# Optimization experiments

Measured on AMD Instinct MI355X. Metric: run time of the kernel, lower is better.

The kernel has to match this reference:

```python
import jax, jax.numpy as jnp
import numpy as np

N_QUBITS = 4
N_LAYERS = 2
BATCH = 524288


def _apply_1q(state, U, axis):
    # state: [B, 2,2,2,2]; U: [2,2] (shared) or [B,2,2] (per-sample); axis = wire index + 1
    s = jnp.moveaxis(state, axis, -1)
    if U.ndim == 3:
        s = jnp.einsum('bij,b...j->b...i', U, s)
    else:
        s = jnp.einsum('ij,...j->...i', U, s)
    return jnp.moveaxis(s, -1, axis)


def _apply_cz(state, a, b):
    # diagonal CZ: flip sign where both qubits are |1>
    sign = jnp.array([[1.0, 1.0], [1.0, -1.0]], dtype=state.dtype)
    shape = [1] * state.ndim
    shape[a] = 2
    shape[b] = 2
    return state * sign.reshape(shape)


def _quantum_expval(feats, w):
    # feats: [B, n_qubits] angles; w: [n_layers, n_qubits, 3] Rot params
    B = feats.shape[0]
    state = jnp.zeros((B,) + (2,) * N_QUBITS, jnp.complex64)
    state = state.at[(slice(None),) + (0,) * N_QUBITS].set(1.0)
    # per-sample RY embedding
    for i in range(N_QUBITS):
        c = jnp.cos(feats[:, i] * 0.5)
        s = jnp.sin(feats[:, i] * 0.5)
        U = jnp.stack([jnp.stack([c, -s], -1), jnp.stack([s, c], -1)], -2).astype(jnp.complex64)
        state = _apply_1q(state, U, i + 1)
    # variational layers: Rot(phi,theta,omega) = RZ(omega) RY(theta) RZ(phi), then CZ chain
    for l in range(N_LAYERS):
        for i in range(N_QUBITS):
            phi, theta, omega = w[l, i, 0], w[l, i, 1], w[l, i, 2]
            ct = jnp.cos(theta * 0.5)
            st = jnp.sin(theta * 0.5)
            U = jnp.stack([
                jnp.stack([jnp.exp(-0.5j * (phi + omega)) * ct, -jnp.exp(0.5j * (phi - omega)) * st]),
                jnp.stack([jnp.exp(-0.5j * (phi - omega)) * st, jnp.exp(0.5j * (phi + omega)) * ct]),
            ]).astype(jnp.complex64)
            state = _apply_1q(state, U, i + 1)
        for i in range(N_QUBITS - 1):
            state = _apply_cz(state, i + 1, i + 2)
    probs = jnp.square(jnp.abs(state))
    p = probs.sum(axis=tuple(range(2, N_QUBITS + 1)))  # marginal of wire 0 -> [B, 2]
    return (p[:, 0] - p[:, 1]).astype(jnp.float32)  # <Z_0>


def setup_inputs() -> dict:
    key = jax.random.key(0)
    ks = jax.random.split(key, 12)
    f = jnp.float32
    return {
        'text': jax.random.normal(ks[0], (BATCH, 16), f),
        'image': jax.random.normal(ks[1], (BATCH, 48), f),
        'tW1': jax.random.normal(ks[2], (16, 32), f) * 0.25,
        'tb1': jnp.zeros((32,), f),
        'tW2': jax.random.normal(ks[3], (32, N_QUBITS), f) * 0.18,
        'tb2': jnp.zeros((N_QUBITS,), f),
        'iW1': jax.random.normal(ks[4], (48, 64), f) * 0.14,
        'ib1': jnp.zeros((64,), f),
        'iW2': jax.random.normal(ks[5], (64, N_QUBITS), f) * 0.125,
        'ib2': jnp.zeros((N_QUBITS,), f),
        'qweights': jax.random.normal(ks[6], (N_LAYERS, N_QUBITS, 3), f),
        'cW1': jax.random.normal(ks[7], (1, 16), f),
        'cb1': jnp.zeros((16,), f),
        'cW2': jax.random.normal(ks[8], (16, 2), f) * 0.25,
        'cb2': jnp.zeros((2,), f),
    }


def reference(text, image, tW1, tb1, tW2, tb2, iW1, ib1, iW2, ib2, qweights, cW1, cb1, cW2, cb2):
    tf = jax.nn.relu(text @ tW1 + tb1) @ tW2 + tb2      # [B, 4]
    imf = jax.nn.relu(image @ iW1 + ib1) @ iW2 + ib2    # [B, 4]
    feats = (tf + imf) * 0.5                             # [B, 4]
    q = _quantum_expval(feats, qweights)                 # [B]
    h = jax.nn.relu(q[:, None] @ cW1 + cb1)              # [B, 16]
    return h @ cW2 + cb2                                 # [B, 2]
```

## Files before the change

### kernel.cpp

```cpp
#include <hip/hip_runtime.h>
#include <math.h>

#define NQ 4
#define NL 2

#define O_IMG 0
#define O_AS  12288
#define O_MRE 12544
#define O_MIM 12800
#define LDS_FLOATS 13056

__global__ __launch_bounds__(256, 4) void qnn_fused(
    const float* __restrict__ text, const float* __restrict__ image,
    const float* __restrict__ tW1, const float* __restrict__ tb1,
    const float* __restrict__ tW2, const float* __restrict__ tb2,
    const float* __restrict__ iW1, const float* __restrict__ ib1,
    const float* __restrict__ iW2, const float* __restrict__ ib2,
    const float* __restrict__ qw,
    const float* __restrict__ cW1, const float* __restrict__ cb1,
    const float* __restrict__ cW2, const float* __restrict__ cb2,
    float* __restrict__ out, int B)
{
    __shared__ __align__(16) float S[LDS_FLOATS];
    const int tid = threadIdx.x;

    {
        const int sbase = blockIdx.x * 256;
        #pragma unroll
        for (int j = 0; j < 12; ++j) {
            int flat = j * 256 + tid;
            int sl = flat / 12;
            int c  = flat - sl * 12;
            int sg = sbase + sl; if (sg >= B) sg = B - 1;
            float4 v = ((const float4*)image)[(size_t)sg * 12 + c];
            *(float4*)&S[O_IMG + sl * 48 + c * 4] = v;
        }
    }

    if (tid < 16) {
        const int j = tid;
        float re[16], im[16];
        #pragma unroll
        for (int b = 0; b < 16; ++b) { re[b] = (b == j) ? 1.f : 0.f; im[b] = 0.f; }
        for (int l = 0; l < NL; ++l) {
            for (int i = 0; i < NQ; ++i) {
                float phi   = qw[(l*NQ + i)*3 + 0];
                float theta = qw[(l*NQ + i)*3 + 1];
                float omega = qw[(l*NQ + i)*3 + 2];
                float ct, st; __sincosf(0.5f*theta, &st, &ct);
                float cap, sap, cam, sam;
                __sincosf(0.5f*(phi + omega), &sap, &cap);
                __sincosf(0.5f*(phi - omega), &sam, &cam);
                float u00r =  cap*ct, u00i = -sap*ct;
                float u01r = -cam*st, u01i = -sam*st;
                float u10r =  cam*st, u10i = -sam*st;
                float u11r =  cap*ct, u11i =  sap*ct;
                int mask = 1 << (3 - i);
                #pragma unroll
                for (int b = 0; b < 16; ++b) {
                    if (b & mask) continue;
                    int b1 = b | mask;
                    float a0r = re[b],  a0i = im[b];
                    float a1r = re[b1], a1i = im[b1];
                    re[b]  = u00r*a0r - u00i*a0i + u01r*a1r - u01i*a1i;
                    im[b]  = u00r*a0i + u00i*a0r + u01r*a1i + u01i*a1r;
                    re[b1] = u10r*a0r - u10i*a0i + u11r*a1r - u11i*a1i;
                    im[b1] = u10r*a0i + u10i*a0r + u11r*a1i + u11i*a1r;
                }
            }
            #pragma unroll
            for (int b = 0; b < 16; ++b) {
                float sgn = 1.f;
                if ((b & 0xC) == 0xC) sgn = -sgn;
                if ((b & 0x6) == 0x6) sgn = -sgn;
                if ((b & 0x3) == 0x3) sgn = -sgn;
                re[b] *= sgn; im[b] *= sgn;
            }
        }
        #pragma unroll
        for (int b = 0; b < 16; ++b) { S[O_MRE + j*16 + b] = re[b]; S[O_MIM + j*16 + b] = im[b]; }
    }
    __syncthreads();
    {
        int j = tid >> 4, k = tid & 15;
        float sacc = 0.f;
        #pragma unroll
        for (int b = 0; b < 16; ++b) {
            float sg = (b & 8) ? -1.f : 1.f;
            sacc += sg * (S[O_MRE + j*16 + b]*S[O_MRE + k*16 + b] +
                          S[O_MIM + j*16 + b]*S[O_MIM + k*16 + b]);
        }
        S[O_AS + tid] = sacc;
    }
    __syncthreads();

    const int s  = blockIdx.x * 256 + tid;
    const int cs = (s < B) ? s : (B - 1);

    float xt[16];
    {
        const float4* tg = (const float4*)(text + (size_t)cs * 16);
        #pragma unroll
        for (int k4 = 0; k4 < 4; ++k4) {
            float4 v = tg[k4];
            xt[4*k4] = v.x; xt[4*k4+1] = v.y; xt[4*k4+2] = v.z; xt[4*k4+3] = v.w;
        }
    }

    float f0 = ib2[0] + tb2[0];
    float f1 = ib2[1] + tb2[1];
    float f2 = ib2[2] + tb2[2];
    float f3 = ib2[3] + tb2[3];

    for (int g = 0; g < 2; ++g) {
        float acc[32];
        #pragma unroll
        for (int j = 0; j < 32; ++j) acc[j] = ib1[g*32 + j];
        #pragma unroll 2
        for (int k4 = 0; k4 < 12; ++k4) {
            float4 xv = *(const float4*)&S[O_IMG + tid*48 + k4*4];
            #pragma unroll
            for (int kk = 0; kk < 4; ++kk) {
                float e = (kk == 0) ? xv.x : (kk == 1) ? xv.y : (kk == 2) ? xv.z : xv.w;
                const float* wr = iW1 + (k4*4 + kk)*64 + g*32;
                #pragma unroll
                for (int j = 0; j < 32; ++j)
                    acc[j] = fmaf(e, wr[j], acc[j]);
            }
        }
        #pragma unroll
        for (int j = 0; j < 32; ++j) {
            float r = fmaxf(acc[j], 0.f);
            const float* w2 = iW2 + (g*32 + j)*4;
            f0 = fmaf(r, w2[0], f0); f1 = fmaf(r, w2[1], f1);
            f2 = fmaf(r, w2[2], f2); f3 = fmaf(r, w2[3], f3);
        }
    }

    for (int g = 0; g < 2; ++g) {
        float acc[16];
        #pragma unroll
        for (int j = 0; j < 16; ++j) acc[j] = tb1[g*16 + j];
        #pragma unroll 4
        for (int k = 0; k < 16; ++k) {
            const float* wr = tW1 + k*32 + g*16;
            float e = xt[k];
            #pragma unroll
            for (int j = 0; j < 16; ++j)
                acc[j] = fmaf(e, wr[j], acc[j]);
        }
        #pragma unroll
        for (int j = 0; j < 16; ++j) {
            float r = fmaxf(acc[j], 0.f);
            const float* w2 = tW2 + (g*16 + j)*4;
            f0 = fmaf(r, w2[0], f0); f1 = fmaf(r, w2[1], f1);
            f2 = fmaf(r, w2[2], f2); f3 = fmaf(r, w2[3], f3);
        }
    }

    float c0,s0v,c1,s1v,c2,s2v,c3,s3v;
    __sincosf(f0 * 0.25f, &s0v, &c0);
    __sincosf(f1 * 0.25f, &s1v, &c1);
    __sincosf(f2 * 0.25f, &s2v, &c2);
    __sincosf(f3 * 0.25f, &s3v, &c3);
    float p01[4] = { c0*c1, c0*s1v, s0v*c1, s0v*s1v };
    float p23[4] = { c2*c3, c2*s3v, s2v*c3, s2v*s3v };
    float psi[16];
    #pragma unroll
    for (int x = 0; x < 4; ++x)
        #pragma unroll
        for (int y = 0; y < 4; ++y)
            psi[x*4+y] = p01[x] * p23[y];

    float q = 0.f;
    #pragma unroll
    for (int j = 0; j < 16; ++j) {
        float row = 0.f;
        #pragma unroll
        for (int k4 = 0; k4 < 4; ++k4) {
            float4 a = *(const float4*)&S[O_AS + j*16 + k4*4];
            row = fmaf(a.x, psi[k4*4+0], row);
            row = fmaf(a.y, psi[k4*4+1], row);
            row = fmaf(a.z, psi[k4*4+2], row);
            row = fmaf(a.w, psi[k4*4+3], row);
        }
        q = fmaf(psi[j], row, q);
    }

    float o0 = cb2[0], o1 = cb2[1];
    #pragma unroll
    for (int j = 0; j < 16; ++j) {
        float h = fmaxf(fmaf(q, cW1[j], cb1[j]), 0.f);
        o0 = fmaf(h, cW2[j*2 + 0], o0);
        o1 = fmaf(h, cW2[j*2 + 1], o1);
    }
    if (s < B) ((float2*)out)[s] = make_float2(o0, o1);
}

extern "C" void kernel_launch(void* const* d_in, const int* in_sizes, int n_in,
                              void* d_out, int out_size, void* d_ws, size_t ws_size,
                              hipStream_t stream)
{
    const float* text  = (const float*)d_in[0];
    const float* image = (const float*)d_in[1];
    const float* tW1   = (const float*)d_in[2];
    const float* tb1   = (const float*)d_in[3];
    const float* tW2   = (const float*)d_in[4];
    const float* tb2   = (const float*)d_in[5];
    const float* iW1   = (const float*)d_in[6];
    const float* ib1   = (const float*)d_in[7];
    const float* iW2   = (const float*)d_in[8];
    const float* ib2   = (const float*)d_in[9];
    const float* qw    = (const float*)d_in[10];
    const float* cW1   = (const float*)d_in[11];
    const float* cb1   = (const float*)d_in[12];
    const float* cW2   = (const float*)d_in[13];
    const float* cb2   = (const float*)d_in[14];

    int B = in_sizes[0] / 16;
    int grid = (B + 255) / 256;

    qnn_fused<<<grid, 256, 0, stream>>>(
        text, image, tW1, tb1, tW2, tb2, iW1, ib1, iW2, ib2,
        qw, cW1, cb1, cW2, cb2, (float*)d_out, B);
}
```

Before: 268.5 us.

## Register-tile MLP across samples and hidden units with LDS-staged weights

Each block now handles 128 samples, and each thread computes a 4-sample by 8-hidden-unit register tile for the image MLP and a 4x4 tile for the text MLP. Weights, biases and padded input tiles are staged in LDS. Partial feature sums are reduced through LDS before half the threads run the quantum and head stages. The aim is to stop every thread streaming all weights from global/scalar memory and to raise FMA-to-load reuse. The cost is more LDS per block, an extra barrier, half the threads idle during the tail, and lower occupancy bounds.

```diff
diff --git a/kernel.cpp b/kernel.cpp
--- a/kernel.cpp
+++ b/kernel.cpp
@@ -4,13 +4,26 @@
 #define NQ 4
 #define NL 2
 
-#define O_IMG 0
-#define O_AS  12288
-#define O_MRE 12544
-#define O_MIM 12800
-#define LDS_FLOATS 13056
-
-__global__ __launch_bounds__(256, 4) void qnn_fused(
+#define O_XI   0
+#define O_XT   6272
+#define O_WI1  8448
+#define O_WI2  11520
+#define O_WT1  11776
+#define O_WT2  12288
+#define O_IB1  12416
+#define O_TB1  12480
+#define O_FB2  12512
+#define O_CW1  12516
+#define O_CB1  12532
+#define O_CW2  12548
+#define O_CB2  12580
+#define O_PT   12584
+#define O_AS   17704
+#define O_MRE  17960
+#define O_MIM  18216
+#define LDS_FLOATS 18472
+
+__global__ __launch_bounds__(256, 2) void qnn_fused(
     const float* __restrict__ text, const float* __restrict__ image,
     const float* __restrict__ tW1, const float* __restrict__ tb1,
     const float* __restrict__ tW2, const float* __restrict__ tb2,
@@ -23,18 +36,43 @@
 {
     __shared__ __align__(16) float S[LDS_FLOATS];
     const int tid = threadIdx.x;
-
-    {
-        const int sbase = blockIdx.x * 256;
-        #pragma unroll
-        for (int j = 0; j < 12; ++j) {
-            int flat = j * 256 + tid;
+    const int blk = blockIdx.x;
+
+    {
+        const float4* img4 = (const float4*)image;
+        #pragma unroll
+        for (int i = 0; i < 6; ++i) {
+            int flat = i * 256 + tid;
             int sl = flat / 12;
-            int c  = flat - sl * 12;
-            int sg = sbase + sl; if (sg >= B) sg = B - 1;
-            float4 v = ((const float4*)image)[(size_t)sg * 12 + c];
-            *(float4*)&S[O_IMG + sl * 48 + c * 4] = v;
-        }
+            int c4 = flat - sl * 12;
+            int sg = blk * 128 + sl; if (sg >= B) sg = B - 1;
+            float4 v = img4[(size_t)sg * 12 + c4];
+            float* d = &S[O_XI + sl * 49 + c4 * 4];
+            d[0] = v.x; d[1] = v.y; d[2] = v.z; d[3] = v.w;
+        }
+        const float4* txt4 = (const float4*)text;
+        #pragma unroll
+        for (int i = 0; i < 2; ++i) {
+            int flat = i * 256 + tid;
+            int sl = flat >> 2;
+            int c4 = flat & 3;
+            int sg = blk * 128 + sl; if (sg >= B) sg = B - 1;
+            float4 v = txt4[(size_t)sg * 4 + c4];
+            float* d = &S[O_XT + sl * 17 + c4 * 4];
+            d[0] = v.x; d[1] = v.y; d[2] = v.z; d[3] = v.w;
+        }
+        #pragma unroll
+        for (int i = 0; i < 12; ++i) S[O_WI1 + i*256 + tid] = iW1[i*256 + tid];
+        S[O_WI2 + tid] = iW2[tid];
+        #pragma unroll
+        for (int i = 0; i < 2; ++i) S[O_WT1 + i*256 + tid] = tW1[i*256 + tid];
+        if (tid < 128) S[O_WT2 + tid] = tW2[tid];
+        if (tid < 64)  S[O_IB1 + tid] = ib1[tid];
+        if (tid < 32)  S[O_TB1 + tid] = tb1[tid];
+        if (tid < 4)   S[O_FB2 + tid] = ib2[tid] + tb2[tid];
+        if (tid < 16) { S[O_CW1 + tid] = cW1[tid]; S[O_CB1 + tid] = cb1[tid]; }
+        if (tid < 32)  S[O_CW2 + tid] = cW2[tid];
+        if (tid < 2)   S[O_CB2 + tid] = cb2[tid];
     }
 
     if (tid < 16) {
@@ -81,6 +119,7 @@
         for (int b = 0; b < 16; ++b) { S[O_MRE + j*16 + b] = re[b]; S[O_MIM + j*16 + b] = im[b]; }
     }
     __syncthreads();
+
     {
         int j = tid >> 4, k = tid & 15;
         float sacc = 0.f;
@@ -92,109 +131,164 @@
         }
         S[O_AS + tid] = sacc;
     }
+
+    const int lane = tid & 63;
+    const int wave = tid >> 6;
+    const int hw   = lane >> 5;
+    const int l5   = lane & 31;
+
+    float part[4][4];
+    #pragma unroll
+    for (int r = 0; r < 4; ++r)
+        #pragma unroll
+        for (int o = 0; o < 4; ++o) part[r][o] = 0.f;
+
+    {
+        const int nb = (wave*2 + hw) * 8;
+        float acc[4][8];
+        #pragma unroll
+        for (int j = 0; j < 8; ++j) {
+            float bv = S[O_IB1 + nb + j];
+            acc[0][j] = bv; acc[1][j] = bv; acc[2][j] = bv; acc[3][j] = bv;
+        }
+        const float* x0p = &S[O_XI + (l5 +  0) * 49];
+        const float* x1p = &S[O_XI + (l5 + 32) * 49];
+        const float* x2p = &S[O_XI + (l5 + 64) * 49];
+        const float* x3p = &S[O_XI + (l5 + 96) * 49];
+        const float* wp  = &S[O_WI1 + nb];
+        #pragma unroll
+        for (int k = 0; k < 48; ++k) {
+            float x0 = x0p[k], x1 = x1p[k], x2 = x2p[k], x3 = x3p[k];
+            float4 wA = *(const float4*)&wp[k*64];
+            float4 wB = *(const float4*)&wp[k*64 + 4];
+            acc[0][0] = fmaf(x0, wA.x, acc[0][0]); acc[0][1] = fmaf(x0, wA.y, acc[0][1]);
+            acc[0][2] = fmaf(x0, wA.z, acc[0][2]); acc[0][3] = fmaf(x0, wA.w, acc[0][3]);
+            acc[0][4] = fmaf(x0, wB.x, acc[0][4]); acc[0][5] = fmaf(x0, wB.y, acc[0][5]);
+            acc[0][6] = fmaf(x0, wB.z, acc[0][6]); acc[0][7] = fmaf(x0, wB.w, acc[0][7]);
+            acc[1][0] = fmaf(x1, wA.x, acc[1][0]); acc[1][1] = fmaf(x1, wA.y, acc[1][1]);
+            acc[1][2] = fmaf(x1, wA.z, acc[1][2]); acc[1][3] = fmaf(x1, wA.w, acc[1][3]);
+            acc[1][4] = fmaf(x1, wB.x, acc[1][4]); acc[1][5] = fmaf(x1, wB.y, acc[1][5]);
+            acc[1][6] = fmaf(x1, wB.z, acc[1][6]); acc[1][7] = fmaf(x1, wB.w, acc[1][7]);
+            acc[2][0] = fmaf(x2, wA.x, acc[2][0]); acc[2][1] = fmaf(x2, wA.y, acc[2][1]);
+            acc[2][2] = fmaf(x2, wA.z, acc[2][2]); acc[2][3] = fmaf(x2, wA.w, acc[2][3]);
+            acc[2][4] = fmaf(x2, wB.x, acc[2][4]); acc[2][5] = fmaf(x2, wB.y, acc[2][5]);
+            acc[2][6] = fmaf(x2, wB.z, acc[2][6]); acc[2][7] = fmaf(x2, wB.w, acc[2][7]);
+            acc[3][0] = fmaf(x3, wA.x, acc[3][0]); acc[3][1] = fmaf(x3, wA.y, acc[3][1]);
+            acc[3][2] = fmaf(x3, wA.z, acc[3][2]); acc[3][3] = fmaf(x3, wA.w, acc[3][3]);
+            acc[3][4] = fmaf(x3, wB.x, acc[3][4]); acc[3][5] = fmaf(x3, wB.y, acc[3][5]);
+            acc[3][6] = fmaf(x3, wB.z, acc[3][6]); acc[3][7] = fmaf(x3, wB.w, acc[3][7]);
+        }
+        #pragma unroll
+        for (int j = 0; j < 8; ++j) {
+            float4 w2 = *(const float4*)&S[O_WI2 + (nb + j) * 4];
+            #pragma unroll
+            for (int r = 0; r < 4; ++r) {
+                float h = fmaxf(acc[r][j], 0.f);
+                part[r][0] = fmaf(h, w2.x, part[r][0]);
+                part[r][1] = fmaf(h, w2.y, part[r][1]);
+                part[r][2] = fmaf(h, w2.z, part[r][2]);
+                part[r][3] = fmaf(h, w2.w, part[r][3]);
+            }
+        }
+    }
+
+    {
+        const int nbt = (wave*2 + hw) * 4;
+        float acc[4][4];
+        #pragma unroll
+        for (int j = 0; j < 4; ++j) {
+            float bv = S[O_TB1 + nbt + j];
+            acc[0][j] = bv; acc[1][j] = bv; acc[2][j] = bv; acc[3][j] = bv;
+        }
+        const float* x0p = &S[O_XT + (l5 +  0) * 17];
+        const float* x1p = &S[O_XT + (l5 + 32) * 17];
+        const float* x2p = &S[O_XT + (l5 + 64) * 17];
+        const float* x3p = &S[O_XT + (l5 + 96) * 17];
+        const float* wp  = &S[O_WT1 + nbt];
+        #pragma unroll
+        for (int k = 0; k < 16; ++k) {
+            float x0 = x0p[k], x1 = x1p[k], x2 = x2p[k], x3 = x3p[k];
+            float4 w = *(const float4*)&wp[k*32];
+            acc[0][0] = fmaf(x0, w.x, acc[0][0]); acc[0][1] = fmaf(x0, w.y, acc[0][1]);
+            acc[0][2] = fmaf(x0, w.z, acc[0][2]); acc[0][3] = fmaf(x0, w.w, acc[0][3]);
+            acc[1][0] = fmaf(x1, w.x, acc[1][0]); acc[1][1] = fmaf(x1, w.y, acc[1][1]);
+            acc[1][2] = fmaf(x1, w.z, acc[1][2]); acc[1][3] = fmaf(x1, w.w, acc[1][3]);
+            acc[2][0] = fmaf(x2, w.x, acc[2][0]); acc[2][1] = fmaf(x2, w.y, acc[2][1]);
+            acc[2][2] = fmaf(x2, w.z, acc[2][2]); acc[2][3] = fmaf(x2, w.w, acc[2][3]);
+            acc[3][0] = fmaf(x3, w.x, acc[3][0]); acc[3][1] = fmaf(x3, w.y, acc[3][1]);
+            acc[3][2] = fmaf(x3, w.z, acc[3][2]); acc[3][3] = fmaf(x3, w.w, acc[3][3]);
+        }
+        #pragma unroll
+        for (int j = 0; j < 4; ++j) {
+            float4 w2 = *(const float4*)&S[O_WT2 + (nbt + j) * 4];
+            #pragma unroll
+            for (int r = 0; r < 4; ++r) {
+                float h = fmaxf(acc[r][j], 0.f);
+                part[r][0] = fmaf(h, w2.x, part[r][0]);
+                part[r][1] = fmaf(h, w2.y, part[r][1]);
+                part[r][2] = fmaf(h, w2.z, part[r][2]);
+                part[r][3] = fmaf(h, w2.w, part[r][3]);
+            }
+        }
+    }
+
+    {
+        const int g = wave*2 + hw;
+        #pragma unroll
+        for (int r = 0; r < 4; ++r) {
+            float* d = &S[O_PT + g*640 + (l5 + 32*r)*5];
+            d[0] = part[r][0]; d[1] = part[r][1]; d[2] = part[r][2]; d[3] = part[r][3];
+        }
+    }
     __syncthreads();
 
-    const int s  = blockIdx.x * 256 + tid;
-    const int cs = (s < B) ? s : (B - 1);
-
-    float xt[16];
-    {
-        const float4* tg = (const float4*)(text + (size_t)cs * 16);
-        #pragma unroll
-        for (int k4 = 0; k4 < 4; ++k4) {
-            float4 v = tg[k4];
-            xt[4*k4] = v.x; xt[4*k4+1] = v.y; xt[4*k4+2] = v.z; xt[4*k4+3] = v.w;
-        }
-    }
-
-    float f0 = ib2[0] + tb2[0];
-    float f1 = ib2[1] + tb2[1];
-    float f2 = ib2[2] + tb2[2];
-    float f3 = ib2[3] + tb2[3];
-
-    for (int g = 0; g < 2; ++g) {
-        float acc[32];
-        #pragma unroll
-        for (int j = 0; j < 32; ++j) acc[j] = ib1[g*32 + j];
-        #pragma unroll 2
-        for (int k4 = 0; k4 < 12; ++k4) {
-            float4 xv = *(const float4*)&S[O_IMG + tid*48 + k4*4];
-            #pragma unroll
-            for (int kk = 0; kk < 4; ++kk) {
-                float e = (kk == 0) ? xv.x : (kk == 1) ? xv.y : (kk == 2) ? xv.z : xv.w;
-                const float* wr = iW1 + (k4*4 + kk)*64 + g*32;
-                #pragma unroll
-                for (int j = 0; j < 32; ++j)
-                    acc[j] = fmaf(e, wr[j], acc[j]);
-            }
-        }
-        #pragma unroll
-        for (int j = 0; j < 32; ++j) {
-            float r = fmaxf(acc[j], 0.f);
-            const float* w2 = iW2 + (g*32 + j)*4;
-            f0 = fmaf(r, w2[0], f0); f1 = fmaf(r, w2[1], f1);
-            f2 = fmaf(r, w2[2], f2); f3 = fmaf(r, w2[3], f3);
-        }
-    }
-
-    for (int g = 0; g < 2; ++g) {
-        float acc[16];
-        #pragma unroll
-        for (int j = 0; j < 16; ++j) acc[j] = tb1[g*16 + j];
-        #pragma unroll 4
-        for (int k = 0; k < 16; ++k) {
-            const float* wr = tW1 + k*32 + g*16;
-            float e = xt[k];
-            #pragma unroll
-            for (int j = 0; j < 16; ++j)
-                acc[j] = fmaf(e, wr[j], acc[j]);
-        }
+    if (tid < 128) {
+        const int s = tid;
+        float f0 = S[O_FB2+0], f1 = S[O_FB2+1], f2 = S[O_FB2+2], f3 = S[O_FB2+3];
+        #pragma unroll
+        for (int g = 0; g < 8; ++g) {
+            const float* p = &S[O_PT + g*640 + s*5];
+            f0 += p[0]; f1 += p[1]; f2 += p[2]; f3 += p[3];
+        }
+        float c0,s0v,c1,s1v,c2,s2v,c3,s3v;
+        __sincosf(f0 * 0.25f, &s0v, &c0);
+        __sincosf(f1 * 0.25f, &s1v, &c1);
+        __sincosf(f2 * 0.25f, &s2v, &c2);
+        __sincosf(f3 * 0.25f, &s3v, &c3);
+        float p01[4] = { c0*c1, c0*s1v, s0v*c1, s0v*s1v };
+        float p23[4] = { c2*c3, c2*s3v, s2v*c3, s2v*s3v };
+        float psi[16];
+        #pragma unroll
+        for (int x = 0; x < 4; ++x)
+            #pragma unroll
+            for (int y = 0; y < 4; ++y)
+                psi[x*4+y] = p01[x] * p23[y];
+
+        float q = 0.f;
         #pragma unroll
         for (int j = 0; j < 16; ++j) {
-            float r = fmaxf(acc[j], 0.f);
-            const float* w2 = tW2 + (g*16 + j)*4;
-            f0 = fmaf(r, w2[0], f0); f1 = fmaf(r, w2[1], f1);
-            f2 = fmaf(r, w2[2], f2); f3 = fmaf(r, w2[3], f3);
-        }
-    }
-
-    float c0,s0v,c1,s1v,c2,s2v,c3,s3v;
-    __sincosf(f0 * 0.25f, &s0v, &c0);
-    __sincosf(f1 * 0.25f, &s1v, &c1);
-    __sincosf(f2 * 0.25f, &s2v, &c2);
-    __sincosf(f3 * 0.25f, &s3v, &c3);
-    float p01[4] = { c0*c1, c0*s1v, s0v*c1, s0v*s1v };
-    float p23[4] = { c2*c3, c2*s3v, s2v*c3, s2v*s3v };
-    float psi[16];
-    #pragma unroll
-    for (int x = 0; x < 4; ++x)
-        #pragma unroll
-        for (int y = 0; y < 4; ++y)
-            psi[x*4+y] = p01[x] * p23[y];
-
-    float q = 0.f;
-    #pragma unroll
-    for (int j = 0; j < 16; ++j) {
-        float row = 0.f;
-        #pragma unroll
-        for (int k4 = 0; k4 < 4; ++k4) {
-            float4 a = *(const float4*)&S[O_AS + j*16 + k4*4];
-            row = fmaf(a.x, psi[k4*4+0], row);
-            row = fmaf(a.y, psi[k4*4+1], row);
-            row = fmaf(a.z, psi[k4*4+2], row);
-            row = fmaf(a.w, psi[k4*4+3], row);
-        }
-        q = fmaf(psi[j], row, q);
-    }
-
-    float o0 = cb2[0], o1 = cb2[1];
-    #pragma unroll
-    for (int j = 0; j < 16; ++j) {
-        float h = fmaxf(fmaf(q, cW1[j], cb1[j]), 0.f);
-        o0 = fmaf(h, cW2[j*2 + 0], o0);
-        o1 = fmaf(h, cW2[j*2 + 1], o1);
-    }
-    if (s < B) ((float2*)out)[s] = make_float2(o0, o1);
+            float row = 0.f;
+            #pragma unroll
+            for (int k4 = 0; k4 < 4; ++k4) {
+                float4 a = *(const float4*)&S[O_AS + j*16 + k4*4];
+                row = fmaf(a.x, psi[k4*4+0], row);
+                row = fmaf(a.y, psi[k4*4+1], row);
+                row = fmaf(a.z, psi[k4*4+2], row);
+                row = fmaf(a.w, psi[k4*4+3], row);
+            }
+            q = fmaf(psi[j], row, q);
+        }
+
+        float o0 = S[O_CB2+0], o1 = S[O_CB2+1];
+        #pragma unroll
+        for (int j = 0; j < 16; ++j) {
+            float h = fmaxf(fmaf(q, S[O_CW1+j], S[O_CB1+j]), 0.f);
+            o0 = fmaf(h, S[O_CW2 + j*2 + 0], o0);
+            o1 = fmaf(h, S[O_CW2 + j*2 + 1], o1);
+        }
+        int sg = blk * 128 + s;
+        if (sg < B) ((float2*)out)[sg] = make_float2(o0, o1);
+    }
 }
 
 extern "C" void kernel_launch(void* const* d_in, const int* in_sizes, int n_in,
@@ -218,7 +312,7 @@
     const float* cb2   = (const float*)d_in[14];
 
     int B = in_sizes[0] / 16;
-    int grid = (B + 255) / 256;
+    int grid = (B + 127) / 128;
 
     qnn_fused<<<grid, 256, 0, stream>>>(
         text, image, tW1, tb1, tW2, tb2, iW1, ib1, iW2, ib2,
```

Result: slower. 286.0 us (+6.5%).
